# Performance work log

Measured on AMD Instinct MI355X. Metric: run time of the kernel, lower is better.

The kernel has to match this reference:

```python
import jax, jax.numpy as jnp
import numpy as np

NN_SIZE = 10          # k for kNN (includes the point itself as its own nearest neighbor)
COS_EPS = 1e-8        # torch.nn.CosineSimilarity eps


def _pairwise_sqdist(p):
    # p: (B,N,3) -> (B,N,N) squared euclidean distances without (B,N,N,3) intermediate
    x2 = jnp.sum(p * p, axis=-1)                      # (B,N)
    inner = jnp.einsum('bnd,bmd->bnm', p, p)          # (B,N,N)
    return x2[:, :, None] + x2[:, None, :] - 2.0 * inner


def _batch_normals(points):
    # points: (B,N,3) -> PCA normals (B,N,3)
    d = _pairwise_sqdist(points)                      # (B,N,N)
    _, idx = jax.lax.top_k(-d, NN_SIZE)               # (B,N,K) indices of k nearest
    nbrs = jax.vmap(lambda p, i: p[i])(points, idx)   # (B,N,K,3) gathered neighborhoods
    centered = nbrs - jnp.mean(nbrs, axis=2, keepdims=True)
    cov = jnp.einsum('bnki,bnkj->bnij', centered, centered) / NN_SIZE  # (B,N,3,3)
    _, vecs = jnp.linalg.eigh(cov)                    # eigenvalues ascending
    return vecs[..., :, 0]                            # eigvec of smallest eigval = normal


def setup_inputs() -> dict:
    key = jax.random.key(0)
    k1, k2 = jax.random.split(key)
    pred = jax.random.normal(k1, (8, 4096, 3), dtype=jnp.float32)
    gt_normals = jax.random.normal(k2, (8, 4096, 3), dtype=jnp.float32)
    return {"pred": pred, "gt_normals": gt_normals}


def reference(pred, gt_normals):
    pred_normals = _batch_normals(pred)                         # (B,N,3)
    dot = jnp.sum(pred_normals * gt_normals, axis=-1)           # (B,N)
    na = jnp.linalg.norm(pred_normals, axis=-1)
    nb = jnp.linalg.norm(gt_normals, axis=-1)
    cos = dot / (jnp.maximum(na, COS_EPS) * jnp.maximum(nb, COS_EPS))
    return jnp.mean(1.0 - cos)
```

## Files before the change

kernel.cpp:

```cpp
#include <hip/hip_runtime.h>
#include <math.h>


#define NPTS   4096
#define KNN    10
#define KEEP   6
#define NBINS  256
#define XLO    (-5.5f)
#define INVBW  (256.0f / 11.0f)
#define W      1536
#define QPB    64
#define NB     512
#define LISTCAP 32768

__device__ __forceinline__ unsigned int umed3(unsigned int a, unsigned int b, unsigned int c) {
    unsigned int r;
    asm("v_med3_u32 %0, %1, %2, %3" : "=v"(r) : "v"(a), "v"(b), "v"(c));
    return r;
}

__device__ __forceinline__ void sift(unsigned int nd[KNN], unsigned int key) {
#pragma unroll
    for (int t = KNN - 1; t >= 1; --t)
        nd[t] = umed3(key, nd[t - 1], nd[t]);
    nd[0] = nd[0] < key ? nd[0] : key;
}

__device__ __forceinline__ void sift6(unsigned int nd[KEEP], unsigned int key) {
#pragma unroll
    for (int t = KEEP - 1; t >= 1; --t)
        nd[t] = umed3(key, nd[t - 1], nd[t]);
    nd[0] = nd[0] < key ? nd[0] : key;
}

__device__ __forceinline__ int xbin(float x) {
    int bin = (int)floorf((x - XLO) * INVBW);
    return bin < 0 ? 0 : (bin > NBINS - 1 ? NBINS - 1 : bin);
}

__device__ float normal_loss3f(const float nbx[KNN], const float nby[KNN],
                               const float nbz[KNN], const float* g3)
{
    float sx = 0.f, sy = 0.f, sz = 0.f;
#pragma unroll
    for (int t = 0; t < KNN; ++t) { sx += nbx[t]; sy += nby[t]; sz += nbz[t]; }
    float mx = sx * 0.1f, my = sy * 0.1f, mz = sz * 0.1f;
    float c00 = 0.f, c01 = 0.f, c02 = 0.f, c11 = 0.f, c12 = 0.f, c22 = 0.f;
#pragma unroll
    for (int t = 0; t < KNN; ++t) {
        float ux = nbx[t] - mx, uy = nby[t] - my, uz = nbz[t] - mz;
        c00 = fmaf(ux, ux, c00);
        c01 = fmaf(ux, uy, c01);
        c02 = fmaf(ux, uz, c02);
        c11 = fmaf(uy, uy, c11);
        c12 = fmaf(uy, uz, c12);
        c22 = fmaf(uz, uz, c22);
    }
    float a00 = c00 * 0.1f, a01 = c01 * 0.1f, a02 = c02 * 0.1f;
    float a11 = c11 * 0.1f, a12 = c12 * 0.1f, a22 = c22 * 0.1f;

    float vx = 1.0f, vy = 0.0f, vz = 0.0f;
    float qd = (a00 + a11 + a22) * (1.0f / 3.0f);
    float p1 = a01 * a01 + a02 * a02 + a12 * a12;
    float b00 = a00 - qd, b11 = a11 - qd, b22 = a22 - qd;
    float p2 = b00 * b00 + b11 * b11 + b22 * b22 + 2.0f * p1;
    if (p2 > 1e-30f) {
        float p   = sqrtf(p2 * (1.0f / 6.0f));
        float inv = 1.0f / p;
        float m00 = b00 * inv, m01 = a01 * inv, m02 = a02 * inv;
        float m11 = b11 * inv, m12 = a12 * inv, m22 = b22 * inv;
        float detB = m00 * (m11 * m22 - m12 * m12)
                   - m01 * (m01 * m22 - m12 * m02)
                   + m02 * (m01 * m12 - m11 * m02);
        float r = 0.5f * detB;
        r = r < -1.0f ? -1.0f : (r > 1.0f ? 1.0f : r);
        float phi  = acosf(r) * (1.0f / 3.0f);
        float eig0 = qd + 2.0f * p * cosf(phi + 2.0943951023931953f);
        float r0x = a00 - eig0, r0y = a01, r0z = a02;
        float r1y = a11 - eig0, r1z = a12;
        float r2z = a22 - eig0;
        float c0x = r0y * r1z - r0z * r1y;
        float c0y = r0z * r0y - r0x * r1z;
        float c0z = r0x * r1y - r0y * r0y;
        float c1x = r0y * r2z - r0z * r1z;
        float c1y = r0z * r0z - r0x * r2z;
        float c1z = r0x * r1z - r0y * r0z;
        float c2x = r1y * r2z - r1z * r1z;
        float c2y = r1z * r0z - r0y * r2z;
        float c2z = r0y * r1z - r1y * r0z;
        float n0 = c0x * c0x + c0y * c0y + c0z * c0z;
        float n1 = c1x * c1x + c1y * c1y + c1z * c1z;
        float n2 = c2x * c2x + c2y * c2y + c2z * c2z;
        float bx, by, bz, bn;
        if (n0 >= n1 && n0 >= n2) { bx = c0x; by = c0y; bz = c0z; bn = n0; }
        else if (n1 >= n2)        { bx = c1x; by = c1y; bz = c1z; bn = n1; }
        else                      { bx = c2x; by = c2y; bz = c2z; bn = n2; }
        if (bn > 1e-30f) {
            float s = rsqrtf(bn);
            vx = bx * s; vy = by * s; vz = bz * s;
        }
    }
    float gx = g3[0], gy = g3[1], gz = g3[2];
    float dotg = vx * gx + vy * gy + vz * gz;
    float na = sqrtf(vx * vx + vy * vy + vz * vz);
    float gn = sqrtf(gx * gx + gy * gy + gz * gz);
    float cs = dotg / (fmaxf(na, 1e-8f) * fmaxf(gn, 1e-8f));
    return 1.0f - cs;
}

__global__ __launch_bounds__(1024) void gtnl_bin(
    const float* __restrict__ pred, float4* __restrict__ wsPts,
    unsigned int* __restrict__ wsBins, unsigned int* __restrict__ wsCnt)
{
    __shared__ unsigned int hist[NBINS];
    __shared__ unsigned int bst[NBINS + 1];

    const int tid = threadIdx.x;
    const int b   = blockIdx.x;
    if (b == 0 && tid == 0) wsCnt[0] = 0;
    const float* src = pred + (size_t)b * NPTS * 3;

    if (tid < NBINS) hist[tid] = 0;
    __syncthreads();

    float px[4], py[4], pz[4];
    int   pb[4], pidx[4];
#pragma unroll
    for (int k = 0; k < 4; ++k) {
        int p = tid + 1024 * k;
        float x = src[3 * p + 0];
        float y = src[3 * p + 1];
        float z = src[3 * p + 2];
        int bin = xbin(x);
        px[k] = x; py[k] = y; pz[k] = z; pb[k] = bin; pidx[k] = p;
        atomicAdd(&hist[bin], 1u);
    }
    __syncthreads();

    if (tid < 64) {
        unsigned s0 = hist[4 * tid + 0], s1 = hist[4 * tid + 1];
        unsigned s2 = hist[4 * tid + 2], s3 = hist[4 * tid + 3];
        unsigned tot = s0 + s1 + s2 + s3;
        unsigned pre = tot;
#pragma unroll
        for (int d = 1; d < 64; d <<= 1) {
            unsigned t = __shfl_up(pre, d, 64);
            if (tid >= d) pre += t;
        }
        unsigned ex = pre - tot;
        bst[4 * tid + 0] = ex;
        bst[4 * tid + 1] = ex + s0;
        bst[4 * tid + 2] = ex + s0 + s1;
        bst[4 * tid + 3] = ex + s0 + s1 + s2;
        if (tid == 63) bst[NBINS] = ex + tot;
    }
    __syncthreads();

    if (tid < NBINS) hist[tid] = bst[tid];
    __syncthreads();

#pragma unroll
    for (int k = 0; k < 4; ++k) {
        unsigned pos = atomicAdd(&hist[pb[k]], 1u);
        wsPts[(size_t)b * NPTS + pos] =
            make_float4(px[k], py[k], pz[k], __uint_as_float((unsigned)pidx[k]));
    }
    if (tid < NBINS) wsBins[b * (NBINS + 1) + tid] = bst[tid];
    if (tid == 0)    wsBins[b * (NBINS + 1) + NBINS] = bst[NBINS];
}

__global__ __launch_bounds__(512, 4) void gtnl_scan(
    const float4* __restrict__ wsPts, const float* __restrict__ gt,
    float* __restrict__ qloss, unsigned int* __restrict__ wsCnt,
    unsigned int* __restrict__ wsList, float* __restrict__ wsThr)
{
    __shared__ float4 pts[W];

    const int tid   = threadIdx.x;
    const int bid   = blockIdx.x;
    const int b     = bid >> 6;
    const int chunk = bid & 63;
    const int qbase = chunk * QPB;
    const int s     = tid & 7;
    const int ql    = tid >> 3;

    int W0 = qbase + QPB / 2 - W / 2;
    W0 = W0 < 0 ? 0 : (W0 > NPTS - W ? NPTS - W : W0);

    const float4* wp = wsPts + (size_t)b * NPTS;
    for (int i = tid; i < W; i += 512) pts[i] = wp[W0 + i];
    __syncthreads();

    const int qpos = qbase + ql;
    const float4 q = pts[qpos - W0];

    unsigned int nd6[KEEP];
#pragma unroll
    for (int t = 0; t < KEEP; ++t) nd6[t] = 0x7F000000u;

    int j = s;
#pragma unroll 8
    for (int t = 0; t < W / 8; ++t, j += 8) {
        float4 c = pts[j];
        float dx = q.x - c.x, dy = q.y - c.y, dz = q.z - c.z;
        float d  = fmaf(dx, dx, fmaf(dy, dy, dz * dz));
        unsigned int key = (__float_as_uint(d) & 0xFFFFF000u) | (unsigned)j;
        sift6(nd6, key);
    }
    const unsigned int kmin6 = nd6[KEEP - 1];

    unsigned int nd[KNN];
#pragma unroll
    for (int t = 0; t < KEEP; ++t) nd[t] = nd6[t];
#pragma unroll
    for (int t = KEEP; t < KNN; ++t) nd[t] = 0x7F000000u;
#pragma unroll
    for (int r = 1; r <= 4; r <<= 1) {
        unsigned int tmp[KNN];
#pragma unroll
        for (int t = 0; t < KNN; ++t) tmp[t] = nd[t];
#pragma unroll
        for (int t = 0; t < KNN; ++t) {
            unsigned int pk = (unsigned int)__shfl_xor((int)tmp[t], r, 64);
            sift(nd, pk);
        }
    }

    unsigned int sok = (kmin6 > nd[KNN - 1]) ? 1u : 0u;
#pragma unroll
    for (int r = 1; r <= 4; r <<= 1) sok &= (unsigned int)__shfl_xor((int)sok, r, 64);

    unsigned int thr_bits = (nd[KNN - 1] & 0xFFFFF000u) + 0x1000u;
    float thr = __uint_as_float(thr_bits);
    float hw  = __uint_as_float(__float_as_uint(sqrtf(thr)) + 4) + 1e-3f;
    bool okL = (W0 == 0)        || (q.x - hw > pts[0].x);
    bool okR = (W0 == NPTS - W) || (q.x + hw < pts[W - 1].x);

    if (okL && okR && sok) {
        float nbx[KNN], nby[KNN], nbz[KNN];
#pragma unroll
        for (int t = 0; t < KNN; ++t) {
            float4 pn = pts[nd[t] & 0xFFFu];
            nbx[t] = pn.x; nby[t] = pn.y; nbz[t] = pn.z;
        }
        const unsigned int qorig = __float_as_uint(q.w);
        float res = normal_loss3f(nbx, nby, nbz, gt + ((size_t)b * NPTS + qorig) * 3);
        if (s == 0) qloss[(size_t)b * NPTS + qpos] = res;
    } else if (s == 0) {
        unsigned int idx = atomicAdd(wsCnt, 1u);
        if (idx < LISTCAP) {
            wsList[idx] = ((unsigned)b << 12) | (unsigned)qpos;
            wsThr[idx]  = hw;
        }
        qloss[(size_t)b * NPTS + qpos] = 0.0f;
    }
}

__global__ __launch_bounds__(256, 4) void gtnl_fix(
    const float4* __restrict__ wsPts, const unsigned int* __restrict__ wsBins,
    const float* __restrict__ gt, float* __restrict__ qloss,
    const unsigned int* __restrict__ wsCnt, const unsigned int* __restrict__ wsList,
    const float* __restrict__ wsThr)
{
    const int lane = threadIdx.x & 63;
    const int wid  = blockIdx.x * 4 + (threadIdx.x >> 6);
    unsigned int n = wsCnt[0];
    n = n < LISTCAP ? n : LISTCAP;

    for (unsigned int i = wid; i < n; i += 4096) {
        unsigned int e = wsList[i];
        const int b    = e >> 12;
        const int qpos = e & 0xFFF;
        const float hw = wsThr[i];
        const float4* wp = wsPts + (size_t)b * NPTS;
        const unsigned int* bst = wsBins + b * (NBINS + 1);

        float4 qv = wp[qpos];
        const unsigned int qorig = __float_as_uint(qv.w);

        const int jlo = (int)bst[xbin(qv.x - hw)];
        const int jhi = (int)bst[xbin(qv.x + hw) + 1];

        unsigned int nd[KNN];
#pragma unroll
        for (int t = 0; t < KNN; ++t) nd[t] = 0x7F000000u;

        for (int j0 = jlo; j0 < jhi; j0 += 64) {
            int j = j0 + lane;
            int js = j < jhi ? j : jhi - 1;
            float4 v = wp[js];
            float dx = qv.x - v.x, dy = qv.y - v.y, dz = qv.z - v.z;
            float d  = fmaf(dx, dx, fmaf(dy, dy, dz * dz));
            unsigned int key = (__float_as_uint(d) & 0xFFFFF000u) | (unsigned)js;
            key = j < jhi ? key : 0xFFFFFFFFu;
            sift(nd, key);
        }

        unsigned int keys[KNN];
#pragma unroll
        for (int r = 0; r < KNN; ++r) {
            unsigned int m = nd[0];
#pragma unroll
            for (int d = 1; d < 64; d <<= 1) {
                unsigned int o = __shfl_xor(m, d, 64);
                m = m < o ? m : o;
            }
            keys[r] = m;
            bool win = (nd[0] == m);
#pragma unroll
            for (int t = 0; t < KNN - 1; ++t) nd[t] = win ? nd[t + 1] : nd[t];
            nd[KNN - 1] = win ? 0xFFFFFFFFu : nd[KNN - 1];
        }

        float nbx[KNN], nby[KNN], nbz[KNN];
#pragma unroll
        for (int t = 0; t < KNN; ++t) {
            float4 pn = wp[keys[t] & 0xFFFu];
            nbx[t] = pn.x; nby[t] = pn.y; nbz[t] = pn.z;
        }
        float res = normal_loss3f(nbx, nby, nbz, gt + ((size_t)b * NPTS + qorig) * 3);
        if (lane == 0) qloss[(size_t)b * NPTS + qpos] = res;
    }
}

__global__ __launch_bounds__(1024) void gtnl_reduceQ(
    const float* __restrict__ qloss, float* __restrict__ out)
{
    __shared__ float sbuf[1024];
    const int tid = threadIdx.x;
    const float4* q4 = (const float4*)qloss;
    float s = 0.0f;
#pragma unroll
    for (int t = 0; t < 8; ++t) {
        float4 v = q4[tid + 1024 * t];
        s += (v.x + v.y) + (v.z + v.w);
    }
    sbuf[tid] = s;
    __syncthreads();
    for (int k = 512; k > 0; k >>= 1) {
        if (tid < k) sbuf[tid] += sbuf[tid + k];
        __syncthreads();
    }
    if (tid == 0) out[0] = sbuf[0] / 32768.0f;
}

__global__ __launch_bounds__(256) void gtnl_brute(
    const float* __restrict__ pred, const float* __restrict__ gt,
    float* __restrict__ partial)
{
    __shared__ float4 ptsB[NPTS];
    __shared__ unsigned int mbuf[64][3][KNN];

    const int tid = threadIdx.x;
    const int b   = blockIdx.x >> 6;
    const int qc  = blockIdx.x & 63;
    const int ql  = tid & 63;
    const int sub = tid >> 6;
    const int qi  = qc * 64 + ql;

    const float* src = pred + (size_t)b * NPTS * 3;
    for (int p = tid; p < NPTS; p += 256) {
        float x = src[3 * p + 0], y = src[3 * p + 1], z = src[3 * p + 2];
        ptsB[p] = make_float4(x, y, z, 0.0f);
    }
    __syncthreads();

    const float4 q = ptsB[qi];
    unsigned int nd[KNN];
#pragma unroll
    for (int t = 0; t < KNN; ++t) nd[t] = 0xFFFFFFFFu;

    const int j0 = sub * 1024;
#pragma unroll 8
    for (int j = j0; j < j0 + 1024; ++j) {
        float4 c = ptsB[j];
        float dx = q.x - c.x, dy = q.y - c.y, dz = q.z - c.z;
        float d  = fmaf(dx, dx, fmaf(dy, dy, dz * dz));
        sift(nd, (__float_as_uint(d) & 0xFFFFF000u) | (unsigned)j);
    }

    if (sub != 0) {
#pragma unroll
        for (int t = 0; t < KNN; ++t) mbuf[ql][sub - 1][t] = nd[t];
    }
    __syncthreads();

    float res = 0.0f;
    if (sub == 0) {
#pragma unroll
        for (int ss = 0; ss < 3; ++ss)
#pragma unroll
            for (int t = 0; t < KNN; ++t) sift(nd, mbuf[ql][ss][t]);
        float nbx[KNN], nby[KNN], nbz[KNN];
#pragma unroll
        for (int t = 0; t < KNN; ++t) {
            float4 pn = ptsB[nd[t] & 0xFFFu];
            nbx[t] = pn.x; nby[t] = pn.y; nbz[t] = pn.z;
        }
        res = normal_loss3f(nbx, nby, nbz, gt + ((size_t)b * NPTS + qi) * 3);
#pragma unroll
        for (int d = 32; d > 0; d >>= 1) res += __shfl_xor(res, d, 64);
    }
    __syncthreads();
    if (tid == 0) partial[blockIdx.x] = res;
}

__global__ __launch_bounds__(512) void gtnl_reduceP(
    const float* __restrict__ partial, float* __restrict__ out)
{
    __shared__ float sb[512];
    const int tid = threadIdx.x;
    sb[tid] = partial[tid];
    __syncthreads();
    for (int k = 256; k > 0; k >>= 1) {
        if (tid < k) sb[tid] += sb[tid + k];
        __syncthreads();
    }
    if (tid == 0) out[0] = sb[0] / 32768.0f;
}

extern "C" void kernel_launch(void* const* d_in, const int* in_sizes, int n_in,
                              void* d_out, int out_size, void* d_ws, size_t ws_size,
                              hipStream_t stream) {
    const float* pred = (const float*)d_in[0];
    const float* gt   = (const float*)d_in[1];
    float* out        = (float*)d_out;

    const size_t PTS_BYTES   = (size_t)8 * NPTS * sizeof(float4);
    const size_t QLOSS_BYTES = (size_t)8 * NPTS * sizeof(float);
    const size_t LIST_BYTES  = (size_t)LISTCAP * sizeof(unsigned);
    const size_t THR_BYTES   = (size_t)LISTCAP * sizeof(float);
    const size_t BINS_BYTES  = (size_t)8 * (NBINS + 1) * sizeof(unsigned);
    const size_t NEED = PTS_BYTES + QLOSS_BYTES + LIST_BYTES + THR_BYTES + BINS_BYTES + 64;

    if (ws_size >= NEED) {
        char* p = (char*)d_ws;
        float4*       wsPts  = (float4*)p;                 p += PTS_BYTES;
        float*        qloss  = (float*)p;                  p += QLOSS_BYTES;
        unsigned int* wsList = (unsigned int*)p;           p += LIST_BYTES;
        float*        wsThr  = (float*)p;                  p += THR_BYTES;
        unsigned int* wsBins = (unsigned int*)p;           p += BINS_BYTES;
        unsigned int* wsCnt  = (unsigned int*)p;

        gtnl_bin<<<8, 1024, 0, stream>>>(pred, wsPts, wsBins, wsCnt);
        gtnl_scan<<<NB, 512, 0, stream>>>(wsPts, gt, qloss, wsCnt, wsList, wsThr);
        gtnl_fix<<<1024, 256, 0, stream>>>(wsPts, wsBins, gt, qloss, wsCnt, wsList, wsThr);
        gtnl_reduceQ<<<1, 1024, 0, stream>>>(qloss, out);
    } else {
        float* partial = (float*)d_ws;
        gtnl_brute<<<512, 256, 0, stream>>>(pred, gt, partial);
        gtnl_reduceP<<<1, 512, 0, stream>>>(partial, out);
    }
}
```

Measured before the change: 54.80 us.

## Fuse fallback kNN search and reduction into scan kernel, drop fix pass

Queries whose local window cannot guarantee correct kNN are now handled inside the scan kernel. The 8-lane group runs a bin-bounded global search directly, instead of appending to a global worklist for a separate fix kernel. Each block also reduces its losses to one partial sum, which replaces the per-query loss array and the single-block reduction. This removes one kernel launch, the atomic worklist and a global round-trip. The cost is warp divergence, because fallback queries now run with only 8 lanes each and stall other queries in the same wavefront.

```diff
diff --git a/kernel.cpp b/kernel.cpp
--- a/kernel.cpp
+++ b/kernel.cpp
@@ -11,7 +11,6 @@
 #define W      1536
 #define QPB    64
 #define NB     512
-#define LISTCAP 32768
 
 __device__ __forceinline__ unsigned int umed3(unsigned int a, unsigned int b, unsigned int c) {
     unsigned int r;
@@ -110,14 +109,13 @@
 
 __global__ __launch_bounds__(1024) void gtnl_bin(
     const float* __restrict__ pred, float4* __restrict__ wsPts,
-    unsigned int* __restrict__ wsBins, unsigned int* __restrict__ wsCnt)
+    unsigned int* __restrict__ wsBins)
 {
     __shared__ unsigned int hist[NBINS];
     __shared__ unsigned int bst[NBINS + 1];
 
     const int tid = threadIdx.x;
     const int b   = blockIdx.x;
-    if (b == 0 && tid == 0) wsCnt[0] = 0;
     const float* src = pred + (size_t)b * NPTS * 3;
 
     if (tid < NBINS) hist[tid] = 0;
@@ -170,11 +168,11 @@
 }
 
 __global__ __launch_bounds__(512, 4) void gtnl_scan(
-    const float4* __restrict__ wsPts, const float* __restrict__ gt,
-    float* __restrict__ qloss, unsigned int* __restrict__ wsCnt,
-    unsigned int* __restrict__ wsList, float* __restrict__ wsThr)
+    const float4* __restrict__ wsPts, const unsigned int* __restrict__ wsBins,
+    const float* __restrict__ gt, float* __restrict__ partial)
 {
     __shared__ float4 pts[W];
+    __shared__ float rbuf[512];
 
     const int tid   = threadIdx.x;
     const int bid   = blockIdx.x;
@@ -235,113 +233,72 @@
     float hw  = __uint_as_float(__float_as_uint(sqrtf(thr)) + 4) + 1e-3f;
     bool okL = (W0 == 0)        || (q.x - hw > pts[0].x);
     bool okR = (W0 == NPTS - W) || (q.x + hw < pts[W - 1].x);
-
-    if (okL && okR && sok) {
-        float nbx[KNN], nby[KNN], nbz[KNN];
+    const bool ok = okL && okR && (sok != 0u);
+
+    if (!ok) {
+        const unsigned int* bst = wsBins + b * (NBINS + 1);
+        const int jlo = (int)bst[xbin(q.x - hw)];
+        const int jhi = (int)bst[xbin(q.x + hw) + 1];
+
+#pragma unroll
+        for (int t = 0; t < KNN; ++t) nd[t] = 0x7F000000u;
+        for (int j0 = jlo + s; j0 < jhi; j0 += 8) {
+            float4 v = wp[j0];
+            float dx = q.x - v.x, dy = q.y - v.y, dz = q.z - v.z;
+            float d  = fmaf(dx, dx, fmaf(dy, dy, dz * dz));
+            sift(nd, (__float_as_uint(d) & 0xFFFFF000u) | (unsigned)j0);
+        }
+#pragma unroll
+        for (int r = 1; r <= 4; r <<= 1) {
+            unsigned int tmp[KNN];
+#pragma unroll
+            for (int t = 0; t < KNN; ++t) tmp[t] = nd[t];
+#pragma unroll
+            for (int t = 0; t < KNN; ++t) {
+                unsigned int pk = (unsigned int)__shfl_xor((int)tmp[t], r, 64);
+                sift(nd, pk);
+            }
+        }
+    }
+
+    float nbx[KNN], nby[KNN], nbz[KNN];
+    if (ok) {
 #pragma unroll
         for (int t = 0; t < KNN; ++t) {
             float4 pn = pts[nd[t] & 0xFFFu];
             nbx[t] = pn.x; nby[t] = pn.y; nbz[t] = pn.z;
         }
-        const unsigned int qorig = __float_as_uint(q.w);
-        float res = normal_loss3f(nbx, nby, nbz, gt + ((size_t)b * NPTS + qorig) * 3);
-        if (s == 0) qloss[(size_t)b * NPTS + qpos] = res;
-    } else if (s == 0) {
-        unsigned int idx = atomicAdd(wsCnt, 1u);
-        if (idx < LISTCAP) {
-            wsList[idx] = ((unsigned)b << 12) | (unsigned)qpos;
-            wsThr[idx]  = hw;
-        }
-        qloss[(size_t)b * NPTS + qpos] = 0.0f;
-    }
-}
-
-__global__ __launch_bounds__(256, 4) void gtnl_fix(
-    const float4* __restrict__ wsPts, const unsigned int* __restrict__ wsBins,
-    const float* __restrict__ gt, float* __restrict__ qloss,
-    const unsigned int* __restrict__ wsCnt, const unsigned int* __restrict__ wsList,
-    const float* __restrict__ wsThr)
-{
-    const int lane = threadIdx.x & 63;
-    const int wid  = blockIdx.x * 4 + (threadIdx.x >> 6);
-    unsigned int n = wsCnt[0];
-    n = n < LISTCAP ? n : LISTCAP;
-
-    for (unsigned int i = wid; i < n; i += 4096) {
-        unsigned int e = wsList[i];
-        const int b    = e >> 12;
-        const int qpos = e & 0xFFF;
-        const float hw = wsThr[i];
-        const float4* wp = wsPts + (size_t)b * NPTS;
-        const unsigned int* bst = wsBins + b * (NBINS + 1);
-
-        float4 qv = wp[qpos];
-        const unsigned int qorig = __float_as_uint(qv.w);
-
-        const int jlo = (int)bst[xbin(qv.x - hw)];
-        const int jhi = (int)bst[xbin(qv.x + hw) + 1];
-
-        unsigned int nd[KNN];
-#pragma unroll
-        for (int t = 0; t < KNN; ++t) nd[t] = 0x7F000000u;
-
-        for (int j0 = jlo; j0 < jhi; j0 += 64) {
-            int j = j0 + lane;
-            int js = j < jhi ? j : jhi - 1;
-            float4 v = wp[js];
-            float dx = qv.x - v.x, dy = qv.y - v.y, dz = qv.z - v.z;
-            float d  = fmaf(dx, dx, fmaf(dy, dy, dz * dz));
-            unsigned int key = (__float_as_uint(d) & 0xFFFFF000u) | (unsigned)js;
-            key = j < jhi ? key : 0xFFFFFFFFu;
-            sift(nd, key);
-        }
-
-        unsigned int keys[KNN];
-#pragma unroll
-        for (int r = 0; r < KNN; ++r) {
-            unsigned int m = nd[0];
-#pragma unroll
-            for (int d = 1; d < 64; d <<= 1) {
-                unsigned int o = __shfl_xor(m, d, 64);
-                m = m < o ? m : o;
-            }
-            keys[r] = m;
-            bool win = (nd[0] == m);
-#pragma unroll
-            for (int t = 0; t < KNN - 1; ++t) nd[t] = win ? nd[t + 1] : nd[t];
-            nd[KNN - 1] = win ? 0xFFFFFFFFu : nd[KNN - 1];
-        }
-
-        float nbx[KNN], nby[KNN], nbz[KNN];
+    } else {
 #pragma unroll
         for (int t = 0; t < KNN; ++t) {
-            float4 pn = wp[keys[t] & 0xFFFu];
+            float4 pn = wp[nd[t] & 0xFFFu];
             nbx[t] = pn.x; nby[t] = pn.y; nbz[t] = pn.z;
         }
-        float res = normal_loss3f(nbx, nby, nbz, gt + ((size_t)b * NPTS + qorig) * 3);
-        if (lane == 0) qloss[(size_t)b * NPTS + qpos] = res;
-    }
-}
-
-__global__ __launch_bounds__(1024) void gtnl_reduceQ(
-    const float* __restrict__ qloss, float* __restrict__ out)
-{
-    __shared__ float sbuf[1024];
+    }
+    const unsigned int qorig = __float_as_uint(q.w);
+    float res = normal_loss3f(nbx, nby, nbz, gt + ((size_t)b * NPTS + qorig) * 3);
+
+    rbuf[tid] = (s == 0) ? res : 0.0f;
+    __syncthreads();
+    for (int k = 256; k > 0; k >>= 1) {
+        if (tid < k) rbuf[tid] += rbuf[tid + k];
+        __syncthreads();
+    }
+    if (tid == 0) partial[bid] = rbuf[0];
+}
+
+__global__ __launch_bounds__(512) void gtnl_reduceP(
+    const float* __restrict__ partial, float* __restrict__ out)
+{
+    __shared__ float sb[512];
     const int tid = threadIdx.x;
-    const float4* q4 = (const float4*)qloss;
-    float s = 0.0f;
-#pragma unroll
-    for (int t = 0; t < 8; ++t) {
-        float4 v = q4[tid + 1024 * t];
-        s += (v.x + v.y) + (v.z + v.w);
-    }
-    sbuf[tid] = s;
-    __syncthreads();
-    for (int k = 512; k > 0; k >>= 1) {
-        if (tid < k) sbuf[tid] += sbuf[tid + k];
+    sb[tid] = partial[tid];
+    __syncthreads();
+    for (int k = 256; k > 0; k >>= 1) {
+        if (tid < k) sb[tid] += sb[tid + k];
         __syncthreads();
     }
-    if (tid == 0) out[0] = sbuf[0] / 32768.0f;
+    if (tid == 0) out[0] = sb[0] / 32768.0f;
 }
 
 __global__ __launch_bounds__(256) void gtnl_brute(
@@ -405,20 +362,6 @@
     if (tid == 0) partial[blockIdx.x] = res;
 }
 
-__global__ __launch_bounds__(512) void gtnl_reduceP(
-    const float* __restrict__ partial, float* __restrict__ out)
-{
-    __shared__ float sb[512];
-    const int tid = threadIdx.x;
-    sb[tid] = partial[tid];
-    __syncthreads();
-    for (int k = 256; k > 0; k >>= 1) {
-        if (tid < k) sb[tid] += sb[tid + k];
-        __syncthreads();
-    }
-    if (tid == 0) out[0] = sb[0] / 32768.0f;
-}
-
 extern "C" void kernel_launch(void* const* d_in, const int* in_sizes, int n_in,
                               void* d_out, int out_size, void* d_ws, size_t ws_size,
                               hipStream_t stream) {
@@ -426,26 +369,20 @@
     const float* gt   = (const float*)d_in[1];
     float* out        = (float*)d_out;
 
-    const size_t PTS_BYTES   = (size_t)8 * NPTS * sizeof(float4);
-    const size_t QLOSS_BYTES = (size_t)8 * NPTS * sizeof(float);
-    const size_t LIST_BYTES  = (size_t)LISTCAP * sizeof(unsigned);
-    const size_t THR_BYTES   = (size_t)LISTCAP * sizeof(float);
-    const size_t BINS_BYTES  = (size_t)8 * (NBINS + 1) * sizeof(unsigned);
-    const size_t NEED = PTS_BYTES + QLOSS_BYTES + LIST_BYTES + THR_BYTES + BINS_BYTES + 64;
+    const size_t PTS_BYTES  = (size_t)8 * NPTS * sizeof(float4);
+    const size_t BINS_BYTES = (size_t)8 * (NBINS + 1) * sizeof(unsigned);
+    const size_t PART_BYTES = (size_t)NB * sizeof(float);
+    const size_t NEED = PTS_BYTES + BINS_BYTES + PART_BYTES;
 
     if (ws_size >= NEED) {
         char* p = (char*)d_ws;
         float4*       wsPts  = (float4*)p;                 p += PTS_BYTES;
-        float*        qloss  = (float*)p;                  p += QLOSS_BYTES;
-        unsigned int* wsList = (unsigned int*)p;           p += LIST_BYTES;
-        float*        wsThr  = (float*)p;                  p += THR_BYTES;
         unsigned int* wsBins = (unsigned int*)p;           p += BINS_BYTES;
-        unsigned int* wsCnt  = (unsigned int*)p;
-
-        gtnl_bin<<<8, 1024, 0, stream>>>(pred, wsPts, wsBins, wsCnt);
-        gtnl_scan<<<NB, 512, 0, stream>>>(wsPts, gt, qloss, wsCnt, wsList, wsThr);
-        gtnl_fix<<<1024, 256, 0, stream>>>(wsPts, wsBins, gt, qloss, wsCnt, wsList, wsThr);
-        gtnl_reduceQ<<<1, 1024, 0, stream>>>(qloss, out);
+        float*        partial= (float*)p;
+
+        gtnl_bin<<<8, 1024, 0, stream>>>(pred, wsPts, wsBins);
+        gtnl_scan<<<NB, 512, 0, stream>>>(wsPts, wsBins, gt, partial);
+        gtnl_reduceP<<<1, NB, 0, stream>>>(partial, out);
     } else {
         float* partial = (float*)d_ws;
         gtnl_brute<<<512, 256, 0, stream>>>(pred, gt, partial);
```

Measured after the change: 108.4 us. 1.98x slower.
